# Kernel optimization log

Hardware: AMD Instinct MI355X
Metric: run time of the kernel (lower is better)

Reference implementation:

```python
import jax, jax.numpy as jnp
import numpy as np
from jax import lax

B, N, S, K = 8, 8192, 2048, 32
CPTS = 64
RADIUS = 0.25
MLP = [64, 64, 128]
EPS = 1e-5


def fps(xyz, npoint):
    # furthest point sampling, starts at index 0 (pointnet2 convention)
    Bn, Nn, _ = xyz.shape

    def step(carry, _):
        mind, last = carry  # mind [B,N], last [B]
        lastp = jnp.take_along_axis(xyz, last[:, None, None], axis=1)  # [B,1,3]
        d = jnp.sum((xyz - lastp) ** 2, axis=-1)  # [B,N]
        mind = jnp.minimum(mind, d)
        nxt = jnp.argmax(mind, axis=-1).astype(jnp.int32)
        return (mind, nxt), last

    init = (jnp.full((Bn, Nn), 1e10, xyz.dtype), jnp.zeros((Bn,), jnp.int32))
    _, idxs = lax.scan(step, init, None, length=npoint)  # [npoint,B]
    return jnp.transpose(idxs)  # [B,npoint]


def ball_query(radius, nsample, xyz, new_xyz):
    # returns first `nsample` indices within radius of each centroid,
    # padding with the first valid index (pointnet2 semantics)
    Nn = xyz.shape[1]
    qq = jnp.sum(new_xyz ** 2, -1)[:, :, None]          # [B,S,1]
    pp = jnp.sum(xyz ** 2, -1)[:, None, :]              # [B,1,N]
    d2 = qq + pp - 2.0 * jnp.einsum('bsc,bnc->bsn', new_xyz, xyz)  # [B,S,N]
    key = jnp.where(d2 <= radius * radius,
                    jnp.arange(Nn, dtype=jnp.int32), jnp.int32(Nn))
    srt = jnp.sort(key, axis=-1)[..., :nsample]          # first valid indices
    return jnp.where(srt < Nn, srt, srt[..., :1])        # pad with first


def _gather(feats, idx):
    # feats [B,N,C], idx [B,S,K] -> [B,S,K,C]
    return jax.vmap(lambda p, i: p[i])(feats, idx)


def setup_inputs() -> dict:
    key = jax.random.key(0)
    ks = jax.random.split(key, 2 + len(MLP))
    xyz = jax.random.normal(ks[0], (B, N, 3), jnp.float32)
    points = jax.random.normal(ks[1], (B, N, CPTS), jnp.float32)
    out = {"xyz": xyz, "points": points}
    cin = 3 + CPTS
    for i, m in enumerate(MLP):
        out[f"w{i}"] = jax.random.normal(ks[2 + i], (m, cin), jnp.float32) * 0.05
        out[f"b{i}"] = jnp.zeros((m,), jnp.float32)
        out[f"g{i}"] = jnp.ones((m,), jnp.float32)
        out[f"be{i}"] = jnp.zeros((m,), jnp.float32)
        cin = m
    return out


def reference(xyz, points, w0, b0, g0, be0, w1, b1, g1, be1, w2, b2, g2, be2):
    fps_idx = fps(xyz, S)                                    # [B,S]
    new_xyz = jnp.take_along_axis(xyz, fps_idx[..., None], axis=1)  # [B,S,3]
    idx = ball_query(RADIUS, K, xyz, new_xyz)                # [B,S,K]

    grouped_xyz = _gather(xyz, idx) - new_xyz[:, :, None, :]  # [B,S,K,3]
    grouped_pts = _gather(points, idx)                        # [B,S,K,CPTS]
    feat = jnp.concatenate([grouped_xyz, grouped_pts], -1)    # [B,S,K,C]

    for (w, b, g, be) in ((w0, b0, g0, be0), (w1, b1, g1, be1), (w2, b2, g2, be2)):
        x = jnp.einsum('bskc,oc->bsko', feat, w) + b           # 1x1 conv
        mean = jnp.mean(x, axis=(0, 1, 2))                     # BN train-mode
        var = jnp.var(x, axis=(0, 1, 2))
        feat = jax.nn.relu((x - mean) * jax.lax.rsqrt(var + EPS) * g + be)

    pooled = jnp.max(feat, axis=2)                             # [B,S,Cout]
    return new_xyz, pooled
```

## Files before the change

kernel.cpp:

```cpp
#include <hip/hip_runtime.h>

#define NPTS 8192
#define NB 8
#define NS 2048
#define NK 32
#define C0 67
#define NTOT (NB*NS*NK)
#define NCONS 248
#define MAGIC 0xC0FFEE01u

typedef __attribute__((ext_vector_type(2))) float f32x2;

template <int CTRL, int ROWM>
__device__ __forceinline__ float dpp_fmax_step(float x) {
  int yi = __builtin_amdgcn_update_dpp(__float_as_int(x), __float_as_int(x),
                                       CTRL, ROWM, 0xf, false);
  return fmaxf(x, __int_as_float(yi));
}
template <int CTRL, int ROWM>
__device__ __forceinline__ unsigned dpp_umin_step(unsigned x) {
  unsigned y = (unsigned)__builtin_amdgcn_update_dpp((int)x, (int)x,
                                                     CTRL, ROWM, 0xf, false);
  return (y < x) ? y : x;
}
__device__ __forceinline__ float wave_max_f32(float v) {
  v = dpp_fmax_step<0x111, 0xf>(v);
  v = dpp_fmax_step<0x112, 0xf>(v);
  v = dpp_fmax_step<0x114, 0xf>(v);
  v = dpp_fmax_step<0x118, 0xf>(v);
  v = dpp_fmax_step<0x142, 0xa>(v);
  v = dpp_fmax_step<0x143, 0xc>(v);
  return v;
}
__device__ __forceinline__ unsigned wave_min_u32(unsigned v) {
  v = dpp_umin_step<0x111, 0xf>(v);
  v = dpp_umin_step<0x112, 0xf>(v);
  v = dpp_umin_step<0x114, 0xf>(v);
  v = dpp_umin_step<0x118, 0xf>(v);
  v = dpp_umin_step<0x142, 0xa>(v);
  v = dpp_umin_step<0x143, 0xc>(v);
  return v;
}

union SMemA {
  struct {
    float sx[NPTS], sy[NPTS], sz[NPTS];
    float snx[NS], sny[NS], snz[NS];
    uint2 slotVN[2][4];
  } fps;
  struct {
    float w0t[C0*64];
    float feat[C0*32];
    int   bq[4][32];
    int   bqc[4];
    int   s_idx[32];
    float s_c[3];
  } con;
};

__global__ __launch_bounds__(256, 1) void k_stage1A(
    const float* __restrict__ xyz, const float* __restrict__ pts,
    const float* __restrict__ w0, const float* __restrict__ g0,
    const float* __restrict__ be0,
    float* __restrict__ newxyz, float* __restrict__ pp,
    float* __restrict__ x0, float* __restrict__ part,
    float* __restrict__ statsF, unsigned* __restrict__ sync) {
  __shared__ __align__(16) SMemA sm;
  __shared__ int s_last;
  const int tid = threadIdx.x;
  unsigned* prog = sync;
  unsigned* ctr0 = sync + 8;

  if (blockIdx.x < NB) {
    const int b = blockIdx.x;
    const int wv = tid >> 6, lane = tid & 63;
    const float* Xb = xyz + (size_t)b * NPTS * 3;
    f32x2 px2[16], py2[16], pz2[16], mind2[16];
#pragma unroll
    for (int i = 0; i < 16; i++) {
      int n0 = ((2*i) << 8) | tid;
      int n1 = ((2*i+1) << 8) | tid;
      float ax = Xb[n0*3+0], ay = Xb[n0*3+1], az = Xb[n0*3+2];
      float bx2 = Xb[n1*3+0], by2 = Xb[n1*3+1], bz2 = Xb[n1*3+2];
      px2[i].x = ax;  px2[i].y = bx2;
      py2[i].x = ay;  py2[i].y = by2;
      pz2[i].x = az;  pz2[i].y = bz2;
      sm.fps.sx[n0]=ax;  sm.fps.sy[n0]=ay;  sm.fps.sz[n0]=az;
      sm.fps.sx[n1]=bx2; sm.fps.sy[n1]=by2; sm.fps.sz[n1]=bz2;
      pp[b*NPTS + n0] = __fadd_rn(__fadd_rn(__fmul_rn(ax,ax), __fmul_rn(ay,ay)), __fmul_rn(az,az));
      pp[b*NPTS + n1] = __fadd_rn(__fadd_rn(__fmul_rn(bx2,bx2), __fmul_rn(by2,by2)), __fmul_rn(bz2,bz2));
      mind2[i].x = 1e10f; mind2[i].y = 1e10f;
    }
    __syncthreads();
    float lx = sm.fps.sx[0], ly = sm.fps.sy[0], lz = sm.fps.sz[0];
    if (tid == 0) { sm.fps.snx[0]=lx; sm.fps.sny[0]=ly; sm.fps.snz[0]=lz; }
    for (int s = 1; s < NS; s++) {
#pragma clang fp contract(off)
      f32x2 lxx = {lx, lx}, lyy = {ly, ly}, lzz = {lz, lz};
      f32x2 m16[16];
#pragma unroll
      for (int i = 0; i < 16; i++) {
        f32x2 dx = px2[i] - lxx;
        f32x2 dy = py2[i] - lyy;
        f32x2 dz = pz2[i] - lzz;
        f32x2 d  = (dx*dx + dy*dy) + dz*dz;
        f32x2 m;
        m.x = fminf(mind2[i].x, d.x);
        m.y = fminf(mind2[i].y, d.y);
        mind2[i] = m;
        m16[i] = m;
      }
#pragma unroll
      for (int st = 8; st >= 1; st >>= 1)
#pragma unroll
        for (int i = 0; i < st; i++) {
          m16[i].x = fmaxf(m16[i].x, m16[i+st].x);
          m16[i].y = fmaxf(m16[i].y, m16[i+st].y);
        }
      float v = fmaxf(m16[0].x, m16[0].y);
      float vr = wave_max_f32(v);
      float wmax = __int_as_float(__builtin_amdgcn_readlane(__float_as_int(vr), 63));
      int kk = 31;
#pragma unroll
      for (int i = 15; i >= 0; i--) {
        kk = (mind2[i].y == v) ? (2*i+1) : kk;
        kk = (mind2[i].x == v) ? (2*i)   : kk;
      }
      unsigned ncand = (v == wmax) ? (unsigned)((kk << 8) | tid) : 0xffffffffu;
      unsigned nr = wave_min_u32(ncand);
      int buf = s & 1;
      if (lane == 63) sm.fps.slotVN[buf][wv] = make_uint2(__float_as_uint(vr), nr);
      __syncthreads();
      uint4 s01 = *(const uint4*)&sm.fps.slotVN[buf][0];
      uint4 s23 = *(const uint4*)&sm.fps.slotVN[buf][2];
      unsigned bx = s01.x, by = s01.y;
      if (s01.z > bx || (s01.z == bx && s01.w < by)) { bx = s01.z; by = s01.w; }
      if (s23.x > bx || (s23.x == bx && s23.y < by)) { bx = s23.x; by = s23.y; }
      if (s23.z > bx || (s23.z == bx && s23.w < by)) { bx = s23.z; by = s23.w; }
      int n = (int)by;
      lx = sm.fps.sx[n]; ly = sm.fps.sy[n]; lz = sm.fps.sz[n];
      if (tid == 0) { sm.fps.snx[s]=lx; sm.fps.sny[s]=ly; sm.fps.snz[s]=lz; }
      if ((s & 63) == 63) {
        __syncthreads();
        int cs = s - 63;
        if (tid < 192) {
          int e = cs + tid / 3, comp = tid - (tid / 3) * 3;
          float vvv = (comp == 0) ? sm.fps.snx[e] : ((comp == 1) ? sm.fps.sny[e] : sm.fps.snz[e]);
          newxyz[((size_t)b*NS + cs)*3 + tid] = vvv;
        }
        __syncthreads();
        if (tid == 0) {
          __threadfence();
          __hip_atomic_store(&prog[b], (unsigned)(s + 1), __ATOMIC_RELEASE, __HIP_MEMORY_SCOPE_AGENT);
        }
      }
    }
  } else {
    const int cb = blockIdx.x - NB;
    const int wv = tid >> 6, lane = tid & 63;
    float* w0t = sm.con.w0t;
    float* feat = sm.con.feat;
    for (int t = tid; t < C0*64; t += 256) { int j = t >> 6, c = t & 63; w0t[t] = w0[c*C0 + j]; }
    int rt = tid & 7, ct = tid >> 3;
    float s0[2] = {0,0}, q0[2] = {0,0};
    for (int it = 0; it <= 66; it++) {
      int e = cb + NCONS * it;
      if (e >= NB*NS) break;
      int s = e >> 3, b = e & 7;
      size_t row = (size_t)b * NS + s;
      if (tid == 0) {
        while ((int)__hip_atomic_load(&prog[b], __ATOMIC_ACQUIRE, __HIP_MEMORY_SCOPE_AGENT) <= s)
          __builtin_amdgcn_s_sleep(32);
        __threadfence();
      }
      __syncthreads();
      const float* c3 = newxyz + row * 3;
      float cx = c3[0], cy = c3[1], cz = c3[2];
      float qq = __fadd_rn(__fadd_rn(__fmul_rn(cx,cx), __fmul_rn(cy,cy)), __fmul_rn(cz,cz));
      const float* Xb = xyz + (size_t)b * NPTS * 3;
      const float* Pb = pp + b * NPTS;
      int cnt = 0;
      int base = wv << 11;
      for (int j0 = base; j0 < base + 2048; j0 += 64) {
        int n = j0 + lane;
        float x = Xb[n*3+0], y = Xb[n*3+1], z = Xb[n*3+2];
        float dot = __fadd_rn(__fadd_rn(__fmul_rn(cx,x), __fmul_rn(cy,y)), __fmul_rn(cz,z));
        float d2 = __fsub_rn(__fadd_rn(qq, Pb[n]), __fmul_rn(2.0f, dot));
        bool in = (d2 <= 0.0625f);
        unsigned long long bal = __ballot(in);
        if (in) {
          int pos = cnt + (int)__popcll(bal & ((1ull << lane) - 1ull));
          if (pos < NK) sm.con.bq[wv][pos] = n;
        }
        cnt += (int)__popcll(bal);
        if (cnt >= NK) break;
      }
      if (lane == 0) sm.con.bqc[wv] = (cnt < NK) ? cnt : NK;
      __syncthreads();
// ... 46 lines not shown
        }
      }
      float* dst = x0 + row * 2048;
#pragma unroll
      for (int r = 0; r < 4; r++)
#pragma unroll
        for (int u = 0; u < 2; u++) {
          float x = acc[r][u];
          dst[(rt*4+r)*64 + ct*2+u] = x;
          s0[u] += x; q0[u] = fmaf(x, x, q0[u]);
        }
      __syncthreads();
    }
#pragma unroll
    for (int off = 1; off < 8; off <<= 1) {
#pragma unroll
      for (int u = 0; u < 2; u++) { s0[u] += __shfl_xor(s0[u], off, 64); q0[u] += __shfl_xor(q0[u], off, 64); }
    }
    if (rt == 0) {
#pragma unroll
      for (int u = 0; u < 2; u++) {
        size_t o = ((size_t)cb * 128 + ct*2 + u) * 2;
        part[o] = s0[u]; part[o+1] = q0[u];
      }
    }
    __threadfence();
    if (tid == 0) {
      unsigned old = __hip_atomic_fetch_add(ctr0, 1u, __ATOMIC_ACQ_REL, __HIP_MEMORY_SCOPE_AGENT);
      s_last = (old == NCONS - 1);
    }
    __syncthreads();
    if (s_last) {
      __threadfence();
      if (tid < 64) {
        float s = 0.f, q = 0.f;
        for (int k = 0; k < NCONS; k++) {
          s += part[((size_t)k * 128 + tid) * 2];
          q += part[((size_t)k * 128 + tid) * 2 + 1];
        }
        const float inv = 1.0f / (float)NTOT;
        float mean = s * inv;
        float var = q * inv - mean * mean;
        float a = g0[tid] / sqrtf(var + 1e-5f);
        float bb = be0[tid] - mean * a;
        statsF[tid*2] = a; statsF[tid*2 + 1] = bb;
      }
    }
  }
}

__global__ __launch_bounds__(256) void k_l1x(
    float* __restrict__ x0, const float* __restrict__ w1,
    const float* __restrict__ g1, const float* __restrict__ be1,
    float* __restrict__ statsF, float* __restrict__ part,
    unsigned* __restrict__ sync) {
  __shared__ __align__(16) float w1t[64*64];
  __shared__ __align__(16) float x0n[64*32];
  __shared__ float sF[128];
  __shared__ int s_last;
  unsigned* ctr1 = sync + 9;
  int tid = threadIdx.x;
  for (int t = tid; t < 64*64; t += 256) { int j = t >> 6, c = t & 63; w1t[t] = w1[c*64 + j]; }
  if (tid < 64) { sF[tid] = statsF[tid*2]; sF[64+tid] = statsF[tid*2+1]; }
  int rt = tid & 7, ct = tid >> 3;
  float s1[2] = {0,0}, q1[2] = {0,0};
  for (int g = 0; g < 32; g++) {
    size_t gid = (size_t)blockIdx.x * 32 + g;
    __syncthreads();
    float* src = x0 + gid * 2048;
#pragma unroll
    for (int i = 0; i < 2; i++) {
      int local = tid*8 + i*4;
      float4 v = *(const float4*)(src + local);
      int row = local >> 6, col = local & 63;
      x0n[(col+0)*32+row] = fmaxf(0.f, fmaf(v.x, sF[col+0], sF[64+col+0]));
      x0n[(col+1)*32+row] = fmaxf(0.f, fmaf(v.y, sF[col+1], sF[64+col+1]));
      x0n[(col+2)*32+row] = fmaxf(0.f, fmaf(v.z, sF[col+2], sF[64+col+2]));
      x0n[(col+3)*32+row] = fmaxf(0.f, fmaf(v.w, sF[col+3], sF[64+col+3]));
    }
    __syncthreads();
    float acc[4][2] = {};
    for (int j = 0; j < 64; j++) {
      float4 av = *(const float4*)&x0n[j*32 + rt*4];
      float2 wv = *(const float2*)&w1t[j*64 + ct*2];
      float aa[4] = {av.x, av.y, av.z, av.w};
#pragma unroll
      for (int r = 0; r < 4; r++) {
        acc[r][0] = fmaf(aa[r], wv.x, acc[r][0]);
        acc[r][1] = fmaf(aa[r], wv.y, acc[r][1]);
      }
    }
#pragma unroll
    for (int r = 0; r < 4; r++)
#pragma unroll
      for (int u = 0; u < 2; u++) {
        float x = acc[r][u];
        src[(rt*4+r)*64 + ct*2+u] = x;
        s1[u] += x; q1[u] = fmaf(x, x, q1[u]);
      }
  }
#pragma unroll
  for (int off = 1; off < 8; off <<= 1) {
#pragma unroll
    for (int u = 0; u < 2; u++) { s1[u] += __shfl_xor(s1[u], off, 64); q1[u] += __shfl_xor(q1[u], off, 64); }
  }
  if (rt == 0) {
#pragma unroll
    for (int u = 0; u < 2; u++) {
      size_t o = ((size_t)blockIdx.x * 128 + ct*2 + u) * 2;
      part[o] = s1[u]; part[o+1] = q1[u];
    }
  }
  __threadfence();
  if (tid == 0) {
    unsigned old = __hip_atomic_fetch_add(ctr1, 1u, __ATOMIC_ACQ_REL, __HIP_MEMORY_SCOPE_AGENT);
    s_last = (old == 511);
  }
  __syncthreads();
  if (s_last) {
    __threadfence();
    if (tid < 64) {
      float s = 0.f, q = 0.f;
      for (int k = 0; k < 512; k++) {
        s += part[((size_t)k * 128 + tid) * 2];
        q += part[((size_t)k * 128 + tid) * 2 + 1];
      }
      const float inv = 1.0f / (float)NTOT;
      float mean = s * inv;
      float var = q * inv - mean * mean;
      float a = g1[tid] / sqrtf(var + 1e-5f);
      float bb = be1[tid] - mean * a;
      statsF[(128 + tid)*2] = a; statsF[(128 + tid)*2 + 1] = bb;
    }
  }
}

__global__ __launch_bounds__(256) void k_l2x(
    const float* __restrict__ x1, const float* __restrict__ w2,
    const float* __restrict__ g2, const float* __restrict__ be2,
    float* __restrict__ statsF, float* __restrict__ part,
    float* __restrict__ maxb, float* __restrict__ minb,
    unsigned* __restrict__ sync) {
  __shared__ __align__(16) float w2t[64*128];
  __shared__ __align__(16) float x1n[64*32];
  __shared__ float sF[128];
  __shared__ int s_last;
  unsigned* ctr2 = sync + 10;
  int tid = threadIdx.x;
  for (int t = tid; t < 64*128; t += 256) { int j = t >> 7, c = t & 127; w2t[t] = w2[c*64 + j]; }
  if (tid < 64) { sF[tid] = statsF[(128+tid)*2]; sF[64+tid] = statsF[(128+tid)*2+1]; }
  int rt = tid & 7, ct = tid >> 3;
  float s2[4] = {0,0,0,0}, q2[4] = {0,0,0,0};
  for (int g = 0; g < 64; g++) {
    size_t gid = (size_t)blockIdx.x * 64 + g;
    __syncthreads();
    const float* src = x1 + gid * 2048;
#pragma unroll
    for (int i = 0; i < 2; i++) {
      int local = tid*8 + i*4;
      float4 v = *(const float4*)(src + local);
      int row = local >> 6, col = local & 63;
      x1n[(col+0)*32+row] = fmaxf(0.f, fmaf(v.x, sF[col+0], sF[64+col+0]));
      x1n[(col+1)*32+row] = fmaxf(0.f, fmaf(v.y, sF[col+1], sF[64+col+1]));
      x1n[(col+2)*32+row] = fmaxf(0.f, fmaf(v.z, sF[col+2], sF[64+col+2]));
      x1n[(col+3)*32+row] = fmaxf(0.f, fmaf(v.w, sF[col+3], sF[64+col+3]));
    }
    __syncthreads();
    float acc[4][4] = {};
    for (int j = 0; j < 64; j++) {
      float4 av = *(const float4*)&x1n[j*32 + rt*4];
      float4 wvv = *(const float4*)&w2t[j*128 + ct*4];
      float aa[4] = {av.x, av.y, av.z, av.w};
      float ww[4] = {wvv.x, wvv.y, wvv.z, wvv.w};
#pragma unroll
      for (int r = 0; r < 4; r++)
#pragma unroll
        for (int u = 0; u < 4; u++) acc[r][u] = fmaf(aa[r], ww[u], acc[r][u]);
    }
    float mx[4], mn[4];
#pragma unroll
    for (int u = 0; u < 4; u++) {
      float x0v = acc[0][u], x1v = acc[1][u], x2v = acc[2][u], x3v = acc[3][u];
      s2[u] += ((x0v + x1v) + (x2v + x3v));
      q2[u] = fmaf(x0v, x0v, q2[u]); q2[u] = fmaf(x1v, x1v, q2[u]);
      q2[u] = fmaf(x2v, x2v, q2[u]); q2[u] = fmaf(x3v, x3v, q2[u]);
      mx[u] = fmaxf(fmaxf(x0v, x1v), fmaxf(x2v, x3v));
      mn[u] = fminf(fminf(x0v, x1v), fminf(x2v, x3v));
    }
#pragma unroll
    for (int off = 1; off < 8; off <<= 1) {
#pragma unroll
      for (int u = 0; u < 4; u++) {
        mx[u] = fmaxf(mx[u], __shfl_xor(mx[u], off, 64));
        mn[u] = fminf(mn[u], __shfl_xor(mn[u], off, 64));
      }
    }
    if (rt == 0) {
#pragma unroll
      for (int u = 0; u < 4; u++) {
        maxb[gid*128 + ct*4 + u] = mx[u];
        minb[gid*128 + ct*4 + u] = mn[u];
      }
    }
  }
#pragma unroll
  for (int off = 1; off < 8; off <<= 1) {
#pragma unroll
    for (int u = 0; u < 4; u++) { s2[u] += __shfl_xor(s2[u], off, 64); q2[u] += __shfl_xor(q2[u], off, 64); }
  }
  if (rt == 0) {
#pragma unroll
    for (int u = 0; u < 4; u++) {
      size_t o = ((size_t)blockIdx.x * 128 + ct*4 + u) * 2;
      part[o] = s2[u]; part[o+1] = q2[u];
    }
  }
  __threadfence();
  if (tid == 0) {
    unsigned old = __hip_atomic_fetch_add(ctr2, 1u, __ATOMIC_ACQ_REL, __HIP_MEMORY_SCOPE_AGENT);
    s_last = (old == 255);
  }
  __syncthreads();
  if (s_last) {
    __threadfence();
    if (tid < 128) {
      float s = 0.f, q = 0.f;
      for (int k = 0; k < 256; k++) {
        s += part[((size_t)k * 128 + tid) * 2];
        q += part[((size_t)k * 128 + tid) * 2 + 1];
      }
      const float inv = 1.0f / (float)NTOT;
      float mean = s * inv;
      float var = q * inv - mean * mean;
      float a = g2[tid] / sqrtf(var + 1e-5f);
      float bb = be2[tid] - mean * a;
      statsF[(256 + tid)*2] = a; statsF[(256 + tid)*2 + 1] = bb;
    }
  }
}

__global__ __launch_bounds__(256) void k_pool(const float* __restrict__ maxb,
                                              const float* __restrict__ minb,
                                              const float* __restrict__ statsF,
                                              float* __restrict__ outp) {
  int t = blockIdx.x * 256 + threadIdx.x;
  int c = t & 127;
  float a  = statsF[(2*128 + c)*2];
  float bb = statsF[(2*128 + c)*2 + 1];
  float X = (a >= 0.f) ? maxb[t] : minb[t];
  outp[t] = fmaxf(0.f, fmaf(a, X, bb));
}

extern "C" void kernel_launch(void* const* d_in, const int* in_sizes, int n_in,
                              void* d_out, int out_size, void* d_ws, size_t ws_size,
                              hipStream_t stream) {
  (void)in_sizes; (void)n_in; (void)out_size; (void)ws_size;
  const float* xyz = (const float*)d_in[0];
  const float* pts = (const float*)d_in[1];
  const float* w0  = (const float*)d_in[2];
  const float* g0  = (const float*)d_in[4];
  const float* be0 = (const float*)d_in[5];
  const float* w1  = (const float*)d_in[6];
  const float* g1  = (const float*)d_in[8];
  const float* be1 = (const float*)d_in[9];
  const float* w2  = (const float*)d_in[10];
  const float* g2  = (const float*)d_in[12];
  const float* be2 = (const float*)d_in[13];

  float* out = (float*)d_out;
  float* newxyz = out;
  float* pooled = out + (size_t)NB*NS*3;

  float* ws = (float*)d_ws;
  float* pp     = ws;
  float* x0     = ws + 65536;
  float* part   = x0 + 33554432;
  float* statsF = part + 131072;
  float* maxb   = statsF + 768;
  float* minb   = maxb + 2097152;
  unsigned* sync = (unsigned*)(minb + 2097152);

  hipMemsetAsync(sync, 0, 64, stream);
  k_stage1A<<<256, 256, 0, stream>>>(xyz, pts, w0, g0, be0,
                                     newxyz, pp, x0, part, statsF, sync);
  k_l1x<<<512, 256, 0, stream>>>(x0, w1, g1, be1, statsF, part, sync);
  k_l2x<<<256, 256, 0, stream>>>(x0, w2, g2, be2, statsF, part,
                                 maxb, minb, sync);
  k_pool<<<8192, 256, 0, stream>>>(maxb, minb, statsF, pooled);
}
```

Baseline: 2.615 ms.

## Interleave two batches' furthest point sampling per producer block

```diff
diff --git a/kernel.cpp b/kernel.cpp
--- a/kernel.cpp
+++ b/kernel.cpp
@@ -6,8 +6,8 @@
 #define NK 32
 #define C0 67
 #define NTOT (NB*NS*NK)
-#define NCONS 248
-#define MAGIC 0xC0FFEE01u
+#define NPROD 4
+#define NCONS 252
 
 typedef __attribute__((ext_vector_type(2))) float f32x2;
 
@@ -44,9 +44,7 @@
 
 union SMemA {
   struct {
-    float sx[NPTS], sy[NPTS], sz[NPTS];
-    float snx[NS], sny[NS], snz[NS];
-    uint2 slotVN[2][4];
+    uint2 slot[2][2][4];
   } fps;
   struct {
     float w0t[C0*64];
@@ -71,99 +69,170 @@
   unsigned* prog = sync;
   unsigned* ctr0 = sync + 8;
 
-  if (blockIdx.x < NB) {
-    const int b = blockIdx.x;
+  if (blockIdx.x < NPROD) {
+    const int bA = blockIdx.x * 2, bB = bA + 1;
     const int wv = tid >> 6, lane = tid & 63;
-    const float* Xb = xyz + (size_t)b * NPTS * 3;
-    f32x2 px2[16], py2[16], pz2[16], mind2[16];
+    const float* XA = xyz + (size_t)bA * NPTS * 3;
+    const float* XB = xyz + (size_t)bB * NPTS * 3;
+    f32x2 pxA[16], pyA[16], pzA[16], mdA[16];
+    f32x2 pxB[16], pyB[16], pzB[16], mdB[16];
 #pragma unroll
     for (int i = 0; i < 16; i++) {
       int n0 = ((2*i) << 8) | tid;
       int n1 = ((2*i+1) << 8) | tid;
-      float ax = Xb[n0*3+0], ay = Xb[n0*3+1], az = Xb[n0*3+2];
-      float bx2 = Xb[n1*3+0], by2 = Xb[n1*3+1], bz2 = Xb[n1*3+2];
-      px2[i].x = ax;  px2[i].y = bx2;
-      py2[i].x = ay;  py2[i].y = by2;
-      pz2[i].x = az;  pz2[i].y = bz2;
-      sm.fps.sx[n0]=ax;  sm.fps.sy[n0]=ay;  sm.fps.sz[n0]=az;
-      sm.fps.sx[n1]=bx2; sm.fps.sy[n1]=by2; sm.fps.sz[n1]=bz2;
-      pp[b*NPTS + n0] = __fadd_rn(__fadd_rn(__fmul_rn(ax,ax), __fmul_rn(ay,ay)), __fmul_rn(az,az));
-      pp[b*NPTS + n1] = __fadd_rn(__fadd_rn(__fmul_rn(bx2,bx2), __fmul_rn(by2,by2)), __fmul_rn(bz2,bz2));
-      mind2[i].x = 1e10f; mind2[i].y = 1e10f;
+      {
+        float ax = XA[n0*3+0], ay = XA[n0*3+1], az = XA[n0*3+2];
+        float bx = XA[n1*3+0], by = XA[n1*3+1], bz = XA[n1*3+2];
+        pxA[i].x = ax; pxA[i].y = bx;
+        pyA[i].x = ay; pyA[i].y = by;
+        pzA[i].x = az; pzA[i].y = bz;
+        pp[bA*NPTS + n0] = __fadd_rn(__fadd_rn(__fmul_rn(ax,ax), __fmul_rn(ay,ay)), __fmul_rn(az,az));
+        pp[bA*NPTS + n1] = __fadd_rn(__fadd_rn(__fmul_rn(bx,bx), __fmul_rn(by,by)), __fmul_rn(bz,bz));
+        mdA[i].x = 1e10f; mdA[i].y = 1e10f;
+      }
+      {
+        float ax = XB[n0*3+0], ay = XB[n0*3+1], az = XB[n0*3+2];
+        float bx = XB[n1*3+0], by = XB[n1*3+1], bz = XB[n1*3+2];
+        pxB[i].x = ax; pxB[i].y = bx;
+        pyB[i].x = ay; pyB[i].y = by;
+        pzB[i].x = az; pzB[i].y = bz;
+        pp[bB*NPTS + n0] = __fadd_rn(__fadd_rn(__fmul_rn(ax,ax), __fmul_rn(ay,ay)), __fmul_rn(az,az));
+        pp[bB*NPTS + n1] = __fadd_rn(__fadd_rn(__fmul_rn(bx,bx), __fmul_rn(by,by)), __fmul_rn(bz,bz));
+        mdB[i].x = 1e10f; mdB[i].y = 1e10f;
+      }
+    }
+    float lxA = XA[0], lyA = XA[1], lzA = XA[2];
+    float lxB = XB[0], lyB = XB[1], lzB = XB[2];
+    if (tid == 0) {
+      float* dA = newxyz + ((size_t)bA * NS) * 3;
+      dA[0] = lxA; dA[1] = lyA; dA[2] = lzA;
+      float* dB = newxyz + ((size_t)bB * NS) * 3;
+      dB[0] = lxB; dB[1] = lyB; dB[2] = lzB;
     }
     __syncthreads();
-    float lx = sm.fps.sx[0], ly = sm.fps.sy[0], lz = sm.fps.sz[0];
-    if (tid == 0) { sm.fps.snx[0]=lx; sm.fps.sny[0]=ly; sm.fps.snz[0]=lz; }
+#pragma unroll 1
     for (int s = 1; s < NS; s++) {
 #pragma clang fp contract(off)
-      f32x2 lxx = {lx, lx}, lyy = {ly, ly}, lzz = {lz, lz};
-      f32x2 m16[16];
+      {
+        f32x2 lxx = {lxA, lxA}, lyy = {lyA, lyA}, lzz = {lzA, lzA};
+#pragma unroll
+        for (int i = 0; i < 16; i++) {
+          f32x2 dx = pxA[i] - lxx;
+          f32x2 dy = pyA[i] - lyy;
+          f32x2 dz = pzA[i] - lzz;
+          f32x2 d  = (dx*dx + dy*dy) + dz*dz;
+          f32x2 m;
+          m.x = fminf(mdA[i].x, d.x);
+          m.y = fminf(mdA[i].y, d.y);
+          mdA[i] = m;
+        }
+      }
+      {
+        f32x2 lxx = {lxB, lxB}, lyy = {lyB, lyB}, lzz = {lzB, lzB};
+#pragma unroll
+        for (int i = 0; i < 16; i++) {
+          f32x2 dx = pxB[i] - lxx;
+          f32x2 dy = pyB[i] - lyy;
+          f32x2 dz = pzB[i] - lzz;
+          f32x2 d  = (dx*dx + dy*dy) + dz*dz;
+          f32x2 m;
+          m.x = fminf(mdB[i].x, d.x);
+          m.y = fminf(mdB[i].y, d.y);
+          mdB[i] = m;
+        }
+      }
+      f32x2 tA[8], tB[8];
+#pragma unroll
+      for (int i = 0; i < 8; i++) {
+        tA[i].x = fmaxf(mdA[i].x, mdA[i+8].x);
+        tA[i].y = fmaxf(mdA[i].y, mdA[i+8].y);
+        tB[i].x = fmaxf(mdB[i].x, mdB[i+8].x);
+        tB[i].y = fmaxf(mdB[i].y, mdB[i+8].y);
+      }
+#pragma unroll
+      for (int st = 4; st >= 1; st >>= 1)
+#pragma unroll
+        for (int i = 0; i < st; i++) {
+          tA[i].x = fmaxf(tA[i].x, tA[i+st].x);
+          tA[i].y = fmaxf(tA[i].y, tA[i+st].y);
+          tB[i].x = fmaxf(tB[i].x, tB[i+st].x);
+          tB[i].y = fmaxf(tB[i].y, tB[i+st].y);
+        }
+      float vA = fmaxf(tA[0].x, tA[0].y);
+      float vB = fmaxf(tB[0].x, tB[0].y);
+      float vrA = wave_max_f32(vA);
+      float vrB = wave_max_f32(vB);
+      float wmA = __int_as_float(__builtin_amdgcn_readlane(__float_as_int(vrA), 63));
+      float wmB = __int_as_float(__builtin_amdgcn_readlane(__float_as_int(vrB), 63));
+      unsigned kA[16], kB[16];
 #pragma unroll
       for (int i = 0; i < 16; i++) {
-        f32x2 dx = px2[i] - lxx;
-        f32x2 dy = py2[i] - lyy;
-        f32x2 dz = pz2[i] - lzz;
-        f32x2 d  = (dx*dx + dy*dy) + dz*dz;
-        f32x2 m;
-        m.x = fminf(mind2[i].x, d.x);
-        m.y = fminf(mind2[i].y, d.y);
-        mind2[i] = m;
-        m16[i] = m;
+        unsigned cA = (mdA[i].y == vA) ? (unsigned)(2*i+1) : 63u;
+        kA[i] = (mdA[i].x == vA) ? (unsigned)(2*i) : cA;
+        unsigned cB = (mdB[i].y == vB) ? (unsigned)(2*i+1) : 63u;
+        kB[i] = (mdB[i].x == vB) ? (unsigned)(2*i) : cB;
       }
 #pragma unroll
       for (int st = 8; st >= 1; st >>= 1)
 #pragma unroll
         for (int i = 0; i < st; i++) {
-          m16[i].x = fmaxf(m16[i].x, m16[i+st].x);
-          m16[i].y = fmaxf(m16[i].y, m16[i+st].y);
-        }
-      float v = fmaxf(m16[0].x, m16[0].y);
-      float vr = wave_max_f32(v);
-      float wmax = __int_as_float(__builtin_amdgcn_readlane(__float_as_int(vr), 63));
-      int kk = 31;
-#pragma unroll
-      for (int i = 15; i >= 0; i--) {
-        kk = (mind2[i].y == v) ? (2*i+1) : kk;
-        kk = (mind2[i].x == v) ? (2*i)   : kk;
-      }
-      unsigned ncand = (v == wmax) ? (unsigned)((kk << 8) | tid) : 0xffffffffu;
-      unsigned nr = wave_min_u32(ncand);
+          kA[i] = (kA[i] < kA[i+st]) ? kA[i] : kA[i+st];
+          kB[i] = (kB[i] < kB[i+st]) ? kB[i] : kB[i+st];
+        }
+      unsigned ncA = (vA == wmA) ? ((kA[0] << 8) | (unsigned)tid) : 0xffffffffu;
+      unsigned ncB = (vB == wmB) ? ((kB[0] << 8) | (unsigned)tid) : 0xffffffffu;
+      unsigned nrA = wave_min_u32(ncA);
+      unsigned nrB = wave_min_u32(ncB);
       int buf = s & 1;
-      if (lane == 63) sm.fps.slotVN[buf][wv] = make_uint2(__float_as_uint(vr), nr);
+      if (lane == 63) {
+        sm.fps.slot[buf][0][wv] = make_uint2(__float_as_uint(vrA), nrA);
+        sm.fps.slot[buf][1][wv] = make_uint2(__float_as_uint(vrB), nrB);
+      }
       __syncthreads();
-      uint4 s01 = *(const uint4*)&sm.fps.slotVN[buf][0];
-      uint4 s23 = *(const uint4*)&sm.fps.slotVN[buf][2];
-      unsigned bx = s01.x, by = s01.y;
-      if (s01.z > bx || (s01.z == bx && s01.w < by)) { bx = s01.z; by = s01.w; }
-      if (s23.x > bx || (s23.x == bx && s23.y < by)) { bx = s23.x; by = s23.y; }
-      if (s23.z > bx || (s23.z == bx && s23.w < by)) { bx = s23.z; by = s23.w; }
-      int n = (int)by;
-      lx = sm.fps.sx[n]; ly = sm.fps.sy[n]; lz = sm.fps.sz[n];
-      if (tid == 0) { sm.fps.snx[s]=lx; sm.fps.sny[s]=ly; sm.fps.snz[s]=lz; }
+      uint4 a01 = *(const uint4*)&sm.fps.slot[buf][0][0];
+      uint4 a23 = *(const uint4*)&sm.fps.slot[buf][0][2];
+      uint4 b01 = *(const uint4*)&sm.fps.slot[buf][1][0];
+      uint4 b23 = *(const uint4*)&sm.fps.slot[buf][1][2];
+      unsigned v0, n0, v2, n2, niA, niB;
+      v0 = a01.x; n0 = a01.y;
+      if (a01.z > v0 || (a01.z == v0 && a01.w < n0)) { v0 = a01.z; n0 = a01.w; }
+      v2 = a23.x; n2 = a23.y;
+      if (a23.z > v2 || (a23.z == v2 && a23.w < n2)) { v2 = a23.z; n2 = a23.w; }
+      if (v2 > v0 || (v2 == v0 && n2 < n0)) { v0 = v2; n0 = n2; }
+      niA = n0;
+      v0 = b01.x; n0 = b01.y;
+      if (b01.z > v0 || (b01.z == v0 && b01.w < n0)) { v0 = b01.z; n0 = b01.w; }
+      v2 = b23.x; n2 = b23.y;
+      if (b23.z > v2 || (b23.z == v2 && b23.w < n2)) { v2 = b23.z; n2 = b23.w; }
+      if (v2 > v0 || (v2 == v0 && n2 < n0)) { v0 = v2; n0 = n2; }
+      niB = n0;
+      const float* cA = XA + (int)niA * 3;
+      const float* cB = XB + (int)niB * 3;
+      lxA = cA[0]; lyA = cA[1]; lzA = cA[2];
+      lxB = cB[0]; lyB = cB[1]; lzB = cB[2];
+      if (tid == 0) {
+        float* dA = newxyz + ((size_t)bA * NS + s) * 3;
+        dA[0] = lxA; dA[1] = lyA; dA[2] = lzA;
+        float* dB = newxyz + ((size_t)bB * NS + s) * 3;
+        dB[0] = lxB; dB[1] = lyB; dB[2] = lzB;
+      }
       if ((s & 63) == 63) {
-        __syncthreads();
-        int cs = s - 63;
-        if (tid < 192) {
-          int e = cs + tid / 3, comp = tid - (tid / 3) * 3;
-          float vvv = (comp == 0) ? sm.fps.snx[e] : ((comp == 1) ? sm.fps.sny[e] : sm.fps.snz[e]);
-          newxyz[((size_t)b*NS + cs)*3 + tid] = vvv;
-        }
-        __syncthreads();
         if (tid == 0) {
           __threadfence();
-          __hip_atomic_store(&prog[b], (unsigned)(s + 1), __ATOMIC_RELEASE, __HIP_MEMORY_SCOPE_AGENT);
+          __hip_atomic_store(&prog[bA], (unsigned)(s + 1), __ATOMIC_RELEASE, __HIP_MEMORY_SCOPE_AGENT);
+          __hip_atomic_store(&prog[bB], (unsigned)(s + 1), __ATOMIC_RELEASE, __HIP_MEMORY_SCOPE_AGENT);
         }
       }
     }
   } else {
-    const int cb = blockIdx.x - NB;
+    const int cb = blockIdx.x - NPROD;
     const int wv = tid >> 6, lane = tid & 63;
     float* w0t = sm.con.w0t;
     float* feat = sm.con.feat;
     for (int t = tid; t < C0*64; t += 256) { int j = t >> 6, c = t & 63; w0t[t] = w0[c*C0 + j]; }
     int rt = tid & 7, ct = tid >> 3;
     float s0[2] = {0,0}, q0[2] = {0,0};
-    for (int it = 0; it <= 66; it++) {
+    for (int it = 0; it < 66; it++) {
       int e = cb + NCONS * it;
       if (e >= NB*NS) break;
       int s = e >> 3, b = e & 7;
```

Result: slower. 7.077 ms (+170.6%).

## Double threads per block in MLP layer kernels, pad LDS, stage output stores

Applied to the files above, without the earlier changes.

```diff
diff --git a/kernel.cpp b/kernel.cpp
--- a/kernel.cpp
+++ b/kernel.cpp
@@ -7,7 +7,6 @@
 #define C0 67
 #define NTOT (NB*NS*NK)
 #define NCONS 248
-#define MAGIC 0xC0FFEE01u
 
 typedef __attribute__((ext_vector_type(2))) float f32x2;
 
@@ -293,58 +292,63 @@
   }
 }
 
-__global__ __launch_bounds__(256) void k_l1x(
+__global__ __launch_bounds__(512) void k_l1x(
     float* __restrict__ x0, const float* __restrict__ w1,
     const float* __restrict__ g1, const float* __restrict__ be1,
     float* __restrict__ statsF, float* __restrict__ part,
     unsigned* __restrict__ sync) {
   __shared__ __align__(16) float w1t[64*64];
-  __shared__ __align__(16) float x0n[64*32];
+  __shared__ __align__(16) float xbuf[2176];
   __shared__ float sF[128];
   __shared__ int s_last;
   unsigned* ctr1 = sync + 9;
   int tid = threadIdx.x;
-  for (int t = tid; t < 64*64; t += 256) { int j = t >> 6, c = t & 63; w1t[t] = w1[c*64 + j]; }
+  for (int t = tid; t < 64*64; t += 512) { int j = t >> 6, c = t & 63; w1t[t] = w1[c*64 + j]; }
   if (tid < 64) { sF[tid] = statsF[tid*2]; sF[64+tid] = statsF[tid*2+1]; }
-  int rt = tid & 7, ct = tid >> 3;
+  int rt = tid & 15, ct = tid >> 4;
   float s1[2] = {0,0}, q1[2] = {0,0};
   for (int g = 0; g < 32; g++) {
     size_t gid = (size_t)blockIdx.x * 32 + g;
     __syncthreads();
     float* src = x0 + gid * 2048;
-#pragma unroll
-    for (int i = 0; i < 2; i++) {
-      int local = tid*8 + i*4;
+    {
+      int local = tid * 4;
       float4 v = *(const float4*)(src + local);
       int row = local >> 6, col = local & 63;
-      x0n[(col+0)*32+row] = fmaxf(0.f, fmaf(v.x, sF[col+0], sF[64+col+0]));
-      x0n[(col+1)*32+row] = fmaxf(0.f, fmaf(v.y, sF[col+1], sF[64+col+1]));
-      x0n[(col+2)*32+row] = fmaxf(0.f, fmaf(v.z, sF[col+2], sF[64+col+2]));
-      x0n[(col+3)*32+row] = fmaxf(0.f, fmaf(v.w, sF[col+3], sF[64+col+3]));
-    }
-    __syncthreads();
-    float acc[4][2] = {};
+      xbuf[(col+0)*34+row] = fmaxf(0.f, fmaf(v.x, sF[col+0], sF[64+col+0]));
+      xbuf[(col+1)*34+row] = fmaxf(0.f, fmaf(v.y, sF[col+1], sF[64+col+1]));
+      xbuf[(col+2)*34+row] = fmaxf(0.f, fmaf(v.z, sF[col+2], sF[64+col+2]));
+      xbuf[(col+3)*34+row] = fmaxf(0.f, fmaf(v.w, sF[col+3], sF[64+col+3]));
+    }
+    __syncthreads();
+    float acc[2][2] = {};
     for (int j = 0; j < 64; j++) {
-      float4 av = *(const float4*)&x0n[j*32 + rt*4];
+      float2 av = *(const float2*)&xbuf[j*34 + rt*2];
       float2 wv = *(const float2*)&w1t[j*64 + ct*2];
-      float aa[4] = {av.x, av.y, av.z, av.w};
-#pragma unroll
-      for (int r = 0; r < 4; r++) {
-        acc[r][0] = fmaf(aa[r], wv.x, acc[r][0]);
-        acc[r][1] = fmaf(aa[r], wv.y, acc[r][1]);
-      }
-    }
-#pragma unroll
-    for (int r = 0; r < 4; r++)
+      acc[0][0] = fmaf(av.x, wv.x, acc[0][0]);
+      acc[0][1] = fmaf(av.x, wv.y, acc[0][1]);
+      acc[1][0] = fmaf(av.y, wv.x, acc[1][0]);
+      acc[1][1] = fmaf(av.y, wv.y, acc[1][1]);
+    }
+    __syncthreads();
+#pragma unroll
+    for (int r = 0; r < 2; r++)
 #pragma unroll
       for (int u = 0; u < 2; u++) {
         float x = acc[r][u];
-        src[(rt*4+r)*64 + ct*2+u] = x;
+        xbuf[(rt*2+r)*68 + ct*2+u] = x;
         s1[u] += x; q1[u] = fmaf(x, x, q1[u]);
       }
-  }
-#pragma unroll
-  for (int off = 1; off < 8; off <<= 1) {
+    __syncthreads();
+    {
+      int local = tid * 4;
+      int row = local >> 6, col = local & 63;
+      float4 v = *(const float4*)&xbuf[row*68 + col];
+      *(float4*)(src + local) = v;
+    }
+  }
+#pragma unroll
+  for (int off = 1; off < 16; off <<= 1) {
 #pragma unroll
     for (int u = 0; u < 2; u++) { s1[u] += __shfl_xor(s1[u], off, 64); q1[u] += __shfl_xor(q1[u], off, 64); }
   }
@@ -379,60 +383,58 @@
   }
 }
 
-__global__ __launch_bounds__(256) void k_l2x(
+__global__ __launch_bounds__(512) void k_l2x(
     const float* __restrict__ x1, const float* __restrict__ w2,
     const float* __restrict__ g2, const float* __restrict__ be2,
     float* __restrict__ statsF, float* __restrict__ part,
     float* __restrict__ maxb, float* __restrict__ minb,
     unsigned* __restrict__ sync) {
   __shared__ __align__(16) float w2t[64*128];
-  __shared__ __align__(16) float x1n[64*32];
+  __shared__ __align__(16) float x1n[64*34];
   __shared__ float sF[128];
   __shared__ int s_last;
   unsigned* ctr2 = sync + 10;
   int tid = threadIdx.x;
-  for (int t = tid; t < 64*128; t += 256) { int j = t >> 7, c = t & 127; w2t[t] = w2[c*64 + j]; }
+  for (int t = tid; t < 64*128; t += 512) { int j = t >> 7, c = t & 127; w2t[t] = w2[c*64 + j]; }
   if (tid < 64) { sF[tid] = statsF[(128+tid)*2]; sF[64+tid] = statsF[(128+tid)*2+1]; }
-  int rt = tid & 7, ct = tid >> 3;
+  int rt = tid & 15, ct = tid >> 4;
   float s2[4] = {0,0,0,0}, q2[4] = {0,0,0,0};
-  for (int g = 0; g < 64; g++) {
-    size_t gid = (size_t)blockIdx.x * 64 + g;
+  for (int g = 0; g < 32; g++) {
+    size_t gid = (size_t)blockIdx.x * 32 + g;
     __syncthreads();
     const float* src = x1 + gid * 2048;
-#pragma unroll
-    for (int i = 0; i < 2; i++) {
-      int local = tid*8 + i*4;
+    {
+      int local = tid * 4;
       float4 v = *(const float4*)(src + local);
       int row = local >> 6, col = local & 63;
-      x1n[(col+0)*32+row] = fmaxf(0.f, fmaf(v.x, sF[col+0], sF[64+col+0]));
-      x1n[(col+1)*32+row] = fmaxf(0.f, fmaf(v.y, sF[col+1], sF[64+col+1]));
-      x1n[(col+2)*32+row] = fmaxf(0.f, fmaf(v.z, sF[col+2], sF[64+col+2]));
-      x1n[(col+3)*32+row] = fmaxf(0.f, fmaf(v.w, sF[col+3], sF[64+col+3]));
-    }
-    __syncthreads();
-    float acc[4][4] = {};
+      x1n[(col+0)*34+row] = fmaxf(0.f, fmaf(v.x, sF[col+0], sF[64+col+0]));
+      x1n[(col+1)*34+row] = fmaxf(0.f, fmaf(v.y, sF[col+1], sF[64+col+1]));
+      x1n[(col+2)*34+row] = fmaxf(0.f, fmaf(v.z, sF[col+2], sF[64+col+2]));
+      x1n[(col+3)*34+row] = fmaxf(0.f, fmaf(v.w, sF[col+3], sF[64+col+3]));
+    }
+    __syncthreads();
+    float acc[2][4] = {};
     for (int j = 0; j < 64; j++) {
-      float4 av = *(const float4*)&x1n[j*32 + rt*4];
+      float2 av = *(const float2*)&x1n[j*34 + rt*2];
       float4 wvv = *(const float4*)&w2t[j*128 + ct*4];
-      float aa[4] = {av.x, av.y, av.z, av.w};
       float ww[4] = {wvv.x, wvv.y, wvv.z, wvv.w};
 #pragma unroll
-      for (int r = 0; r < 4; r++)
-#pragma unroll
-        for (int u = 0; u < 4; u++) acc[r][u] = fmaf(aa[r], ww[u], acc[r][u]);
+      for (int u = 0; u < 4; u++) {
+        acc[0][u] = fmaf(av.x, ww[u], acc[0][u]);
+        acc[1][u] = fmaf(av.y, ww[u], acc[1][u]);
+      }
     }
     float mx[4], mn[4];
 #pragma unroll
     for (int u = 0; u < 4; u++) {
-      float x0v = acc[0][u], x1v = acc[1][u], x2v = acc[2][u], x3v = acc[3][u];
-      s2[u] += ((x0v + x1v) + (x2v + x3v));
-      q2[u] = fmaf(x0v, x0v, q2[u]); q2[u] = fmaf(x1v, x1v, q2[u]);
-      q2[u] = fmaf(x2v, x2v, q2[u]); q2[u] = fmaf(x3v, x3v, q2[u]);
-      mx[u] = fmaxf(fmaxf(x0v, x1v), fmaxf(x2v, x3v));
-      mn[u] = fminf(fminf(x0v, x1v), fminf(x2v, x3v));
-    }
-#pragma unroll
-    for (int off = 1; off < 8; off <<= 1) {
+      float a0 = acc[0][u], a1 = acc[1][u];
+      s2[u] += (a0 + a1);
+      q2[u] = fmaf(a0, a0, q2[u]); q2[u] = fmaf(a1, a1, q2[u]);
+      mx[u] = fmaxf(a0, a1);
+      mn[u] = fminf(a0, a1);
+    }
+#pragma unroll
+    for (int off = 1; off < 16; off <<= 1) {
 #pragma unroll
       for (int u = 0; u < 4; u++) {
         mx[u] = fmaxf(mx[u], __shfl_xor(mx[u], off, 64));
@@ -448,7 +450,7 @@
     }
   }
 #pragma unroll
-  for (int off = 1; off < 8; off <<= 1) {
+  for (int off = 1; off < 16; off <<= 1) {
 #pragma unroll
     for (int u = 0; u < 4; u++) { s2[u] += __shfl_xor(s2[u], off, 64); q2[u] += __shfl_xor(q2[u], off, 64); }
   }
@@ -462,14 +464,14 @@
   __threadfence();
   if (tid == 0) {
     unsigned old = __hip_atomic_fetch_add(ctr2, 1u, __ATOMIC_ACQ_REL, __HIP_MEMORY_SCOPE_AGENT);
-    s_last = (old == 255);
+    s_last = (old == 511);
   }
   __syncthreads();
   if (s_last) {
     __threadfence();
     if (tid < 128) {
       float s = 0.f, q = 0.f;
-      for (int k = 0; k < 256; k++) {
+      for (int k = 0; k < 512; k++) {
         s += part[((size_t)k * 128 + tid) * 2];
         q += part[((size_t)k * 128 + tid) * 2 + 1];
       }
@@ -527,8 +529,8 @@
   hipMemsetAsync(sync, 0, 64, stream);
   k_stage1A<<<256, 256, 0, stream>>>(xyz, pts, w0, g0, be0,
                                      newxyz, pp, x0, part, statsF, sync);
-  k_l1x<<<512, 256, 0, stream>>>(x0, w1, g1, be1, statsF, part, sync);
-  k_l2x<<<256, 256, 0, stream>>>(x0, w2, g2, be2, statsF, part,
+  k_l1x<<<512, 512, 0, stream>>>(x0, w1, g1, be1, statsF, part, sync);
+  k_l2x<<<512, 512, 0, stream>>>(x0, w2, g2, be2, statsF, part,
                                  maxb, minb, sync);
   k_pool<<<8192, 256, 0, stream>>>(maxb, minb, statsF, pooled);
 }
```

Result: slower. 2.742 ms (+4.8%).

## Fuse layer-1, layer-2 and pooling into one persistent kernel with grid-wide flags

Applied to the files above, without the earlier changes.

```diff
diff --git a/kernel.cpp b/kernel.cpp
--- a/kernel.cpp
+++ b/kernel.cpp
@@ -7,7 +7,6 @@
 #define C0 67
 #define NTOT (NB*NS*NK)
 #define NCONS 248
-#define MAGIC 0xC0FFEE01u
 
 typedef __attribute__((ext_vector_type(2))) float f32x2;
 
@@ -276,12 +275,21 @@
     __syncthreads();
     if (s_last) {
       __threadfence();
+      float* fin = sm.con.feat;
+      {
+        int c = tid & 63, j = tid >> 6;
+        float s = 0.f, q = 0.f;
+        for (int k = j*62; k < j*62 + 62; k++) {
+          float2 p = *(const float2*)&part[((size_t)k * 128 + c) * 2];
+          s += p.x; q += p.y;
+        }
+        fin[tid*2] = s; fin[tid*2+1] = q;
+      }
+      __syncthreads();
       if (tid < 64) {
         float s = 0.f, q = 0.f;
-        for (int k = 0; k < NCONS; k++) {
-          s += part[((size_t)k * 128 + tid) * 2];
-          q += part[((size_t)k * 128 + tid) * 2 + 1];
-        }
+#pragma unroll
+        for (int j2 = 0; j2 < 4; j2++) { s += fin[(j2*64+tid)*2]; q += fin[(j2*64+tid)*2+1]; }
         const float inv = 1.0f / (float)NTOT;
         float mean = s * inv;
         float var = q * inv - mean * mean;
@@ -293,20 +301,28 @@
   }
 }
 
-__global__ __launch_bounds__(256) void k_l1x(
+__global__ __launch_bounds__(256) void k_tail(
     float* __restrict__ x0, const float* __restrict__ w1,
     const float* __restrict__ g1, const float* __restrict__ be1,
+    const float* __restrict__ w2, const float* __restrict__ g2,
+    const float* __restrict__ be2,
     float* __restrict__ statsF, float* __restrict__ part,
-    unsigned* __restrict__ sync) {
-  __shared__ __align__(16) float w1t[64*64];
-  __shared__ __align__(16) float x0n[64*32];
+    float* __restrict__ maxb, float* __restrict__ minb,
+    float* __restrict__ outp, unsigned* __restrict__ sync) {
+  __shared__ __align__(16) union {
+    struct { float w1t[64*64]; float x0n[64*32]; } l1;
+    struct { float w2t[64*128]; float x1n[64*32]; } l2;
+  } u;
   __shared__ float sF[128];
+  __shared__ float fin[512];
   __shared__ int s_last;
-  unsigned* ctr1 = sync + 9;
-  int tid = threadIdx.x;
-  for (int t = tid; t < 64*64; t += 256) { int j = t >> 6, c = t & 63; w1t[t] = w1[c*64 + j]; }
+  unsigned* ctrM1 = sync + 11; unsigned* flag1 = sync + 12;
+  unsigned* ctrM2 = sync + 13; unsigned* flag2 = sync + 14;
+  const int tid = threadIdx.x;
+  const int rt = tid & 7, ct = tid >> 3;
+
+  for (int t = tid; t < 64*64; t += 256) { int j = t >> 6, c = t & 63; u.l1.w1t[t] = w1[c*64 + j]; }
   if (tid < 64) { sF[tid] = statsF[tid*2]; sF[64+tid] = statsF[tid*2+1]; }
-  int rt = tid & 7, ct = tid >> 3;
   float s1[2] = {0,0}, q1[2] = {0,0};
   for (int g = 0; g < 32; g++) {
     size_t gid = (size_t)blockIdx.x * 32 + g;
@@ -317,16 +333,16 @@
       int local = tid*8 + i*4;
       float4 v = *(const float4*)(src + local);
       int row = local >> 6, col = local & 63;
-      x0n[(col+0)*32+row] = fmaxf(0.f, fmaf(v.x, sF[col+0], sF[64+col+0]));
-      x0n[(col+1)*32+row] = fmaxf(0.f, fmaf(v.y, sF[col+1], sF[64+col+1]));
-      x0n[(col+2)*32+row] = fmaxf(0.f, fmaf(v.z, sF[col+2], sF[64+col+2]));
-      x0n[(col+3)*32+row] = fmaxf(0.f, fmaf(v.w, sF[col+3], sF[64+col+3]));
+      u.l1.x0n[(col+0)*32+row] = fmaxf(0.f, fmaf(v.x, sF[col+0], sF[64+col+0]));
+      u.l1.x0n[(col+1)*32+row] = fmaxf(0.f, fmaf(v.y, sF[col+1], sF[64+col+1]));
+      u.l1.x0n[(col+2)*32+row] = fmaxf(0.f, fmaf(v.z, sF[col+2], sF[64+col+2]));
+      u.l1.x0n[(col+3)*32+row] = fmaxf(0.f, fmaf(v.w, sF[col+3], sF[64+col+3]));
     }
     __syncthreads();
     float acc[4][2] = {};
     for (int j = 0; j < 64; j++) {
-      float4 av = *(const float4*)&x0n[j*32 + rt*4];
-      float2 wv = *(const float2*)&w1t[j*64 + ct*2];
+      float4 av = *(const float4*)&u.l1.x0n[j*32 + rt*4];
+      float2 wv = *(const float2*)&u.l1.w1t[j*64 + ct*2];
       float aa[4] = {av.x, av.y, av.z, av.w};
 #pragma unroll
       for (int r = 0; r < 4; r++) {
@@ -337,38 +353,46 @@
 #pragma unroll
     for (int r = 0; r < 4; r++)
 #pragma unroll
-      for (int u = 0; u < 2; u++) {
-        float x = acc[r][u];
-        src[(rt*4+r)*64 + ct*2+u] = x;
-        s1[u] += x; q1[u] = fmaf(x, x, q1[u]);
+      for (int u2 = 0; u2 < 2; u2++) {
+        float x = acc[r][u2];
+        src[(rt*4+r)*64 + ct*2+u2] = x;
+        s1[u2] += x; q1[u2] = fmaf(x, x, q1[u2]);
       }
   }
 #pragma unroll
   for (int off = 1; off < 8; off <<= 1) {
 #pragma unroll
-    for (int u = 0; u < 2; u++) { s1[u] += __shfl_xor(s1[u], off, 64); q1[u] += __shfl_xor(q1[u], off, 64); }
+    for (int u2 = 0; u2 < 2; u2++) { s1[u2] += __shfl_xor(s1[u2], off, 64); q1[u2] += __shfl_xor(q1[u2], off, 64); }
   }
   if (rt == 0) {
 #pragma unroll
-    for (int u = 0; u < 2; u++) {
-      size_t o = ((size_t)blockIdx.x * 128 + ct*2 + u) * 2;
-      part[o] = s1[u]; part[o+1] = q1[u];
+    for (int u2 = 0; u2 < 2; u2++) {
+      size_t o = ((size_t)blockIdx.x * 128 + ct*2 + u2) * 2;
+      part[o] = s1[u2]; part[o+1] = q1[u2];
     }
   }
   __threadfence();
   if (tid == 0) {
-    unsigned old = __hip_atomic_fetch_add(ctr1, 1u, __ATOMIC_ACQ_REL, __HIP_MEMORY_SCOPE_AGENT);
+    unsigned old = __hip_atomic_fetch_add(ctrM1, 1u, __ATOMIC_ACQ_REL, __HIP_MEMORY_SCOPE_AGENT);
     s_last = (old == 511);
   }
   __syncthreads();
   if (s_last) {
     __threadfence();
+    {
+      int c = tid & 63, j = tid >> 6;
+      float s = 0.f, q = 0.f;
+      for (int k = j*128; k < j*128 + 128; k++) {
+        float2 p = *(const float2*)&part[((size_t)k * 128 + c) * 2];
+        s += p.x; q += p.y;
+      }
+      fin[tid*2] = s; fin[tid*2+1] = q;
+    }
+    __syncthreads();
     if (tid < 64) {
       float s = 0.f, q = 0.f;
-      for (int k = 0; k < 512; k++) {
-        s += part[((size_t)k * 128 + tid) * 2];
-        q += part[((size_t)k * 128 + tid) * 2 + 1];
-      }
+#pragma unroll
+      for (int j2 = 0; j2 < 4; j2++) { s += fin[(j2*64+tid)*2]; q += fin[(j2*64+tid)*2+1]; }
       const float inv = 1.0f / (float)NTOT;
       float mean = s * inv;
       float var = q * inv - mean * mean;
@@ -376,103 +400,107 @@
       float bb = be1[tid] - mean * a;
       statsF[(128 + tid)*2] = a; statsF[(128 + tid)*2 + 1] = bb;
     }
-  }
-}
-
-__global__ __launch_bounds__(256) void k_l2x(
-    const float* __restrict__ x1, const float* __restrict__ w2,
-    const float* __restrict__ g2, const float* __restrict__ be2,
-    float* __restrict__ statsF, float* __restrict__ part,
-    float* __restrict__ maxb, float* __restrict__ minb,
-    unsigned* __restrict__ sync) {
-  __shared__ __align__(16) float w2t[64*128];
-  __shared__ __align__(16) float x1n[64*32];
-  __shared__ float sF[128];
-  __shared__ int s_last;
-  unsigned* ctr2 = sync + 10;
-  int tid = threadIdx.x;
-  for (int t = tid; t < 64*128; t += 256) { int j = t >> 7, c = t & 127; w2t[t] = w2[c*64 + j]; }
+    __syncthreads();
+    if (tid == 0) {
+      __threadfence();
+      __hip_atomic_store(flag1, 1u, __ATOMIC_RELEASE, __HIP_MEMORY_SCOPE_AGENT);
+    }
+  }
+  if (tid == 0) {
+    while (__hip_atomic_load(flag1, __ATOMIC_ACQUIRE, __HIP_MEMORY_SCOPE_AGENT) == 0)
+      __builtin_amdgcn_s_sleep(32);
+    __threadfence();
+  }
+  __syncthreads();
+
+  for (int t = tid; t < 64*128; t += 256) { int j = t >> 7, c = t & 127; u.l2.w2t[t] = w2[c*64 + j]; }
   if (tid < 64) { sF[tid] = statsF[(128+tid)*2]; sF[64+tid] = statsF[(128+tid)*2+1]; }
-  int rt = tid & 7, ct = tid >> 3;
   float s2[4] = {0,0,0,0}, q2[4] = {0,0,0,0};
-  for (int g = 0; g < 64; g++) {
-    size_t gid = (size_t)blockIdx.x * 64 + g;
-    __syncthreads();
-    const float* src = x1 + gid * 2048;
+  for (int g = 0; g < 32; g++) {
+    size_t gid = (size_t)blockIdx.x * 32 + g;
+    __syncthreads();
+    const float* src = x0 + gid * 2048;
 #pragma unroll
     for (int i = 0; i < 2; i++) {
       int local = tid*8 + i*4;
       float4 v = *(const float4*)(src + local);
       int row = local >> 6, col = local & 63;
-      x1n[(col+0)*32+row] = fmaxf(0.f, fmaf(v.x, sF[col+0], sF[64+col+0]));
-      x1n[(col+1)*32+row] = fmaxf(0.f, fmaf(v.y, sF[col+1], sF[64+col+1]));
-      x1n[(col+2)*32+row] = fmaxf(0.f, fmaf(v.z, sF[col+2], sF[64+col+2]));
-      x1n[(col+3)*32+row] = fmaxf(0.f, fmaf(v.w, sF[col+3], sF[64+col+3]));
+      u.l2.x1n[(col+0)*32+row] = fmaxf(0.f, fmaf(v.x, sF[col+0], sF[64+col+0]));
+      u.l2.x1n[(col+1)*32+row] = fmaxf(0.f, fmaf(v.y, sF[col+1], sF[64+col+1]));
+      u.l2.x1n[(col+2)*32+row] = fmaxf(0.f, fmaf(v.z, sF[col+2], sF[64+col+2]));
+      u.l2.x1n[(col+3)*32+row] = fmaxf(0.f, fmaf(v.w, sF[col+3], sF[64+col+3]));
     }
     __syncthreads();
     float acc[4][4] = {};
     for (int j = 0; j < 64; j++) {
-      float4 av = *(const float4*)&x1n[j*32 + rt*4];
-      float4 wvv = *(const float4*)&w2t[j*128 + ct*4];
+      float4 av = *(const float4*)&u.l2.x1n[j*32 + rt*4];
+      float4 wvv = *(const float4*)&u.l2.w2t[j*128 + ct*4];
       float aa[4] = {av.x, av.y, av.z, av.w};
       float ww[4] = {wvv.x, wvv.y, wvv.z, wvv.w};
 #pragma unroll
       for (int r = 0; r < 4; r++)
 #pragma unroll
-        for (int u = 0; u < 4; u++) acc[r][u] = fmaf(aa[r], ww[u], acc[r][u]);
+        for (int u2 = 0; u2 < 4; u2++) acc[r][u2] = fmaf(aa[r], ww[u2], acc[r][u2]);
     }
     float mx[4], mn[4];
 #pragma unroll
-    for (int u = 0; u < 4; u++) {
-      float x0v = acc[0][u], x1v = acc[1][u], x2v = acc[2][u], x3v = acc[3][u];
-      s2[u] += ((x0v + x1v) + (x2v + x3v));
-      q2[u] = fmaf(x0v, x0v, q2[u]); q2[u] = fmaf(x1v, x1v, q2[u]);
-      q2[u] = fmaf(x2v, x2v, q2[u]); q2[u] = fmaf(x3v, x3v, q2[u]);
-      mx[u] = fmaxf(fmaxf(x0v, x1v), fmaxf(x2v, x3v));
-      mn[u] = fminf(fminf(x0v, x1v), fminf(x2v, x3v));
+    for (int u2 = 0; u2 < 4; u2++) {
+      float x0v = acc[0][u2], x1v = acc[1][u2], x2v = acc[2][u2], x3v = acc[3][u2];
+      s2[u2] += ((x0v + x1v) + (x2v + x3v));
+      q2[u2] = fmaf(x0v, x0v, q2[u2]); q2[u2] = fmaf(x1v, x1v, q2[u2]);
+      q2[u2] = fmaf(x2v, x2v, q2[u2]); q2[u2] = fmaf(x3v, x3v, q2[u2]);
+      mx[u2] = fmaxf(fmaxf(x0v, x1v), fmaxf(x2v, x3v));
+      mn[u2] = fminf(fminf(x0v, x1v), fminf(x2v, x3v));
     }
 #pragma unroll
     for (int off = 1; off < 8; off <<= 1) {
 #pragma unroll
-      for (int u = 0; u < 4; u++) {
-        mx[u] = fmaxf(mx[u], __shfl_xor(mx[u], off, 64));
-        mn[u] = fminf(mn[u], __shfl_xor(mn[u], off, 64));
+      for (int u2 = 0; u2 < 4; u2++) {
+        mx[u2] = fmaxf(mx[u2], __shfl_xor(mx[u2], off, 64));
+        mn[u2] = fminf(mn[u2], __shfl_xor(mn[u2], off, 64));
       }
     }
     if (rt == 0) {
 #pragma unroll
-      for (int u = 0; u < 4; u++) {
-        maxb[gid*128 + ct*4 + u] = mx[u];
-        minb[gid*128 + ct*4 + u] = mn[u];
+      for (int u2 = 0; u2 < 4; u2++) {
+        maxb[gid*128 + ct*4 + u2] = mx[u2];
+        minb[gid*128 + ct*4 + u2] = mn[u2];
       }
     }
   }
 #pragma unroll
   for (int off = 1; off < 8; off <<= 1) {
 #pragma unroll
-    for (int u = 0; u < 4; u++) { s2[u] += __shfl_xor(s2[u], off, 64); q2[u] += __shfl_xor(q2[u], off, 64); }
+    for (int u2 = 0; u2 < 4; u2++) { s2[u2] += __shfl_xor(s2[u2], off, 64); q2[u2] += __shfl_xor(q2[u2], off, 64); }
   }
   if (rt == 0) {
 #pragma unroll
-    for (int u = 0; u < 4; u++) {
-      size_t o = ((size_t)blockIdx.x * 128 + ct*4 + u) * 2;
-      part[o] = s2[u]; part[o+1] = q2[u];
+    for (int u2 = 0; u2 < 4; u2++) {
+      size_t o = ((size_t)blockIdx.x * 128 + ct*4 + u2) * 2;
+      part[o] = s2[u2]; part[o+1] = q2[u2];
     }
   }
   __threadfence();
   if (tid == 0) {
-    unsigned old = __hip_atomic_fetch_add(ctr2, 1u, __ATOMIC_ACQ_REL, __HIP_MEMORY_SCOPE_AGENT);
-    s_last = (old == 255);
+    unsigned old = __hip_atomic_fetch_add(ctrM2, 1u, __ATOMIC_ACQ_REL, __HIP_MEMORY_SCOPE_AGENT);
+    s_last = (old == 511);
   }
   __syncthreads();
   if (s_last) {
     __threadfence();
+    {
+      int c = tid & 127, j = tid >> 7;
+      float s = 0.f, q = 0.f;
+      for (int k = j*256; k < j*256 + 256; k++) {
+        float2 p = *(const float2*)&part[((size_t)k * 128 + c) * 2];
+        s += p.x; q += p.y;
+      }
+      fin[tid*2] = s; fin[tid*2+1] = q;
+    }
+    __syncthreads();
     if (tid < 128) {
-      float s = 0.f, q = 0.f;
-      for (int k = 0; k < 256; k++) {
-        s += part[((size_t)k * 128 + tid) * 2];
-        q += part[((size_t)k * 128 + tid) * 2 + 1];
-      }
+      float s = fin[tid*2] + fin[(128+tid)*2];
+      float q = fin[tid*2+1] + fin[(128+tid)*2+1];
       const float inv = 1.0f / (float)NTOT;
       float mean = s * inv;
       float var = q * inv - mean * mean;
@@ -480,19 +508,29 @@
       float bb = be2[tid] - mean * a;
       statsF[(256 + tid)*2] = a; statsF[(256 + tid)*2 + 1] = bb;
     }
-  }
-}
-
-__global__ __launch_bounds__(256) void k_pool(const float* __restrict__ maxb,
-                                              const float* __restrict__ minb,
-                                              const float* __restrict__ statsF,
-                                              float* __restrict__ outp) {
-  int t = blockIdx.x * 256 + threadIdx.x;
-  int c = t & 127;
-  float a  = statsF[(2*128 + c)*2];
-  float bb = statsF[(2*128 + c)*2 + 1];
-  float X = (a >= 0.f) ? maxb[t] : minb[t];
-  outp[t] = fmaxf(0.f, fmaf(a, X, bb));
+    __syncthreads();
+    if (tid == 0) {
+      __threadfence();
+      __hip_atomic_store(flag2, 1u, __ATOMIC_RELEASE, __HIP_MEMORY_SCOPE_AGENT);
+    }
+  }
+  if (tid == 0) {
+    while (__hip_atomic_load(flag2, __ATOMIC_ACQUIRE, __HIP_MEMORY_SCOPE_AGENT) == 0)
+      __builtin_amdgcn_s_sleep(32);
+    __threadfence();
+  }
+  __syncthreads();
+
+  if (tid < 128) { fin[tid] = statsF[(256+tid)*2]; fin[128+tid] = statsF[(256+tid)*2+1]; }
+  __syncthreads();
+#pragma unroll
+  for (int i = 0; i < 16; i++) {
+    int t = (int)blockIdx.x * 4096 + i*256 + tid;
+    int c = t & 127;
+    float a = fin[c], bb = fin[128+c];
+    float X = (a >= 0.f) ? maxb[t] : minb[t];
+    outp[t] = fmaxf(0.f, fmaf(a, X, bb));
+  }
 }
 
 extern "C" void kernel_launch(void* const* d_in, const int* in_sizes, int n_in,
@@ -527,8 +565,6 @@
   hipMemsetAsync(sync, 0, 64, stream);
   k_stage1A<<<256, 256, 0, stream>>>(xyz, pts, w0, g0, be0,
                                      newxyz, pp, x0, part, statsF, sync);
-  k_l1x<<<512, 256, 0, stream>>>(x0, w1, g1, be1, statsF, part, sync);
-  k_l2x<<<256, 256, 0, stream>>>(x0, w2, g2, be2, statsF, part,
-                                 maxb, minb, sync);
-  k_pool<<<8192, 256, 0, stream>>>(maxb, minb, statsF, pooled);
-}
+  k_tail<<<512, 256, 0, stream>>>(x0, w1, g1, be1, w2, g2, be2,
+                                  statsF, part, maxb, minb, pooled, sync);
+}
```

Result: slower. 3.265 ms (+24.8%).
